# Kernel tuning notes

Hardware: AMD Instinct MI355X
Metric: run time of the kernel (lower is better)

## Reference

```python
import jax, jax.numpy as jnp
import numpy as np

N = 8192
C_IN = 512
C_INTER = 128  # in_channels // unit_nums = 512 // 4


def setup_inputs() -> dict:
    key = jax.random.key(0)
    ks = jax.random.split(key, 6)
    x = jax.random.normal(ks[0], (N, C_IN), dtype=jnp.float32)
    # Linear weights init: normal(0, 0.01); biases zero. Stored as [in, out].
    Wg = 0.01 * jax.random.normal(ks[1], (C_IN, C_INTER), dtype=jnp.float32)
    Wt = 0.01 * jax.random.normal(ks[2], (C_IN, C_INTER), dtype=jnp.float32)
    Wp = 0.01 * jax.random.normal(ks[3], (C_IN, C_INTER), dtype=jnp.float32)
    bg = jnp.zeros((C_INTER,), dtype=jnp.float32)
    bt = jnp.zeros((C_INTER,), dtype=jnp.float32)
    bp = jnp.zeros((C_INTER,), dtype=jnp.float32)
    # 1x1 conv weight (1, 2*C_INTER, 1, 1) flattened: first half hits theta, second half phi
    wcat = 0.01 * jax.random.normal(ks[4], (2 * C_INTER,), dtype=jnp.float32)
    return {"x": x, "Wg": Wg, "bg": bg, "Wt": Wt, "bt": bt, "Wp": Wp, "bp": bp, "wcat": wcat}


def reference(x, Wg, bg, Wt, bt, Wp, bp, wcat):
    n = x.shape[0]
    g_x = x @ Wg + bg          # [N, C_inter]
    theta = x @ Wt + bt        # [N, C_inter]
    phi = x @ Wp + bp          # [N, C_inter]
    c = theta.shape[1]
    # 1x1 conv over cat([theta_i, phi_j]) == w1.theta_i + w2.phi_j (outer sum), then ReLU
    a = theta @ wcat[:c]       # [N]
    b = phi @ wcat[c:]         # [N]
    f = jax.nn.relu(a[:, None] + b[None, :])  # [N, N]
    z = (f / n) @ g_x          # [N, C_inter]
    return z
```

## Files before the change

### kernel.cpp

```cpp
#include <hip/hip_runtime.h>

#define C_IN   512
#define C_INT  128
#define NBUCK  8192
#define SEG    32
#define NSEG   256

typedef short short8 __attribute__((ext_vector_type(8)));
typedef float floatx4 __attribute__((ext_vector_type(4)));


__device__ __forceinline__ int bucket_of(float v, float bmin, float inv_w) {
    float fk = (v - bmin) * inv_w;
    fk = fminf(fmaxf(fk, 0.f), (float)(NBUCK - 1));
    return (int)fk;
}

__device__ __forceinline__ short bf16rnd(float v) {
    unsigned u = __float_as_uint(v);
    return (short)((u + 0x7fffu + ((u >> 16) & 1u)) >> 16);
}


__global__ __launch_bounds__(256) void prep_kernel(
        const float* __restrict__ Wt, const float* __restrict__ Wp,
        const float* __restrict__ Wg, const float* __restrict__ wcat,
        const float* __restrict__ bt, const float* __restrict__ bp,
        float* __restrict__ ut, float* __restrict__ up, float* __restrict__ scal,
        unsigned short* __restrict__ WgT) {
    int t = threadIdx.x, bk = blockIdx.x;
    if (bk < 16) {
        const float* W  = (bk < 8) ? Wt : Wp;
        const float* wv = wcat + ((bk < 8) ? 0 : C_INT);
        float* dst      = (bk < 8) ? ut : up;
        int k = (bk & 7) * 64 + (t >> 2);
        int q = t & 3;
        const float4* row = (const float4*)(W + (size_t)k * C_INT);
        const float4* cv4 = (const float4*)wv;
        float s = 0.f;
        #pragma unroll
        for (int i = 0; i < 8; ++i) {
            float4 a = row[q * 8 + i];
            float4 c = cv4[q * 8 + i];
            s += a.x * c.x + a.y * c.y + a.z * c.z + a.w * c.w;
        }
        s += __shfl_xor(s, 1);
        s += __shfl_xor(s, 2);
        if (q == 0) dst[k] = s;
    } else if (bk == 16) {
        float s1p = (t < C_INT) ? bt[t] * wcat[t] : 0.f;
        float s2p = (t < C_INT) ? bp[t] * wcat[C_INT + t] : 0.f;
        for (int off = 32; off; off >>= 1) {
            s1p += __shfl_down(s1p, off);
            s2p += __shfl_down(s2p, off);
        }
        __shared__ float red[8];
        int w = t >> 6, lane = t & 63;
        if (lane == 0) { red[w] = s1p; red[4 + w] = s2p; }
        __syncthreads();
        if (t == 0) {
            scal[0] = red[0] + red[1] + red[2] + red[3];
            scal[1] = red[4] + red[5] + red[6] + red[7];
        }
    } else {
        __shared__ float tile[64][132];
        int kb = (bk - 17) * 64;
        #pragma unroll
        for (int it = 0; it < 8; ++it) {
            int idx = it * 256 + t;
            int r = idx >> 5, c4 = idx & 31;
            *(float4*)&tile[r][c4 * 4] =
                ((const float4*)(Wg + (size_t)(kb + r) * C_INT))[c4];
        }
        __syncthreads();
        int n = t & 127, kc = (t >> 7) * 32;
        unsigned pk[16];
        #pragma unroll
        for (int i = 0; i < 16; ++i) {
            unsigned lo = (unsigned short)bf16rnd(tile[kc + 2 * i][n]);
            unsigned hi = (unsigned short)bf16rnd(tile[kc + 2 * i + 1][n]);
            pk[i] = lo | (hi << 16);
        }
        uint4* dst = (uint4*)(WgT + (size_t)n * C_IN + kb + kc);
        #pragma unroll
        for (int i2 = 0; i2 < 4; ++i2) dst[i2] = *(uint4*)&pk[i2 * 4];
    }
}


#define RSTR 66

__global__ __launch_bounds__(256) void gemm_mfma(
        const float* __restrict__ x, const unsigned short* __restrict__ WgT,
        const float* __restrict__ bg,
        const float* __restrict__ ut, const float* __restrict__ up,
        const float* __restrict__ scal,
        _Float16* __restrict__ g, float* __restrict__ a, float* __restrict__ b) {
    __shared__ float red[3][20][RSTR];
    int tid = threadIdx.x;
    int lane = tid & 63, wv = tid >> 6;
    int bx = blockIdx.x;
    int i0 = (bx >> 1) * 16;
    int cg = bx & 1;
    int m = lane & 15, q = lane >> 4;
    floatx4 accg[4] = {};
    floatx4 accab = {};
    const float* xrow = x + (size_t)(i0 + m) * C_IN + q * 8;
    const float* absrc = (m == 0) ? ut : up;
    #pragma unroll
    for (int ks = 0; ks < 4; ++ks) {
        int k0 = (wv * 4 + ks) * 32;
        float4 f0 = *(const float4*)(xrow + k0);
        float4 f1 = *(const float4*)(xrow + k0 + 4);
        short8 af;
        af[0] = bf16rnd(f0.x); af[1] = bf16rnd(f0.y);
        af[2] = bf16rnd(f0.z); af[3] = bf16rnd(f0.w);
        af[4] = bf16rnd(f1.x); af[5] = bf16rnd(f1.y);
        af[6] = bf16rnd(f1.z); af[7] = bf16rnd(f1.w);
        if (cg == 0) {
            short8 abf = {};
            if (m < 2) {
                float4 u0 = *(const float4*)(absrc + k0 + q * 8);
                float4 u1 = *(const float4*)(absrc + k0 + q * 8 + 4);
                abf[0] = bf16rnd(u0.x); abf[1] = bf16rnd(u0.y);
                abf[2] = bf16rnd(u0.z); abf[3] = bf16rnd(u0.w);
                abf[4] = bf16rnd(u1.x); abf[5] = bf16rnd(u1.y);
                abf[6] = bf16rnd(u1.z); abf[7] = bf16rnd(u1.w);
            }
            accab = __builtin_amdgcn_mfma_f32_16x16x32_bf16(af, abf, accab, 0, 0, 0);
        }
        #pragma unroll
        for (int f = 0; f < 4; ++f) {
            short8 bfr = *(const short8*)(WgT + (size_t)(cg * 64 + f * 16 + m) * C_IN + k0 + q * 8);
            accg[f] = __builtin_amdgcn_mfma_f32_16x16x32_bf16(af, bfr, accg[f], 0, 0, 0);
        }
    }
    if (wv) {
        #pragma unroll
        for (int f = 0; f < 4; ++f)
            #pragma unroll
            for (int r = 0; r < 4; ++r)
                red[wv - 1][f * 4 + r][lane] = accg[f][r];
        #pragma unroll
        for (int r = 0; r < 4; ++r)
            red[wv - 1][16 + r][lane] = accab[r];
    }
    __syncthreads();
    if (wv == 0) {
        #pragma unroll
        for (int w = 0; w < 3; ++w) {
            #pragma unroll
            for (int f = 0; f < 4; ++f)
                #pragma unroll
                for (int r = 0; r < 4; ++r)
                    accg[f][r] += red[w][f * 4 + r][lane];
            #pragma unroll
            for (int r = 0; r < 4; ++r)
                accab[r] += red[w][16 + r][lane];
        }
        #pragma unroll
        for (int f = 0; f < 4; ++f) {
            int col = cg * 64 + f * 16 + m;
            float bgv = bg[col];
            #pragma unroll
            for (int r = 0; r < 4; ++r) {
                int row = i0 + q * 4 + r;
                g[(size_t)row * C_INT + col] = (_Float16)(accg[f][r] + bgv);
            }
        }
        if (cg == 0 && m < 2) {
            float off = m ? scal[1] : scal[0];
            float* dst = m ? b : a;
            #pragma unroll
            for (int r = 0; r < 4; ++r) dst[i0 + q * 4 + r] = accab[r] + off;
        }
    }
}


__global__ __launch_bounds__(1024) void sort_kernel(
        const float* __restrict__ b, float* __restrict__ scal,
        unsigned* __restrict__ offs_g, unsigned short* __restrict__ perm_g,
        float* __restrict__ bsort_g) {
    __shared__ unsigned oh[NBUCK / 2];
    __shared__ unsigned cur[NBUCK / 2];
    __shared__ unsigned short ls[8192];
    __shared__ unsigned wtu[16];
    __shared__ float smn[16], smx[16], sbp[2];
    int t = threadIdx.x, lane = t & 63, wv = t >> 6;
    #pragma unroll
    for (int r = 0; r < 4; ++r) { oh[t + r * 1024] = 0u; cur[t + r * 1024] = 0u; }
    float bv[8];
    float mn = 1e30f, mx = -1e30f;
    #pragma unroll
    for (int r = 0; r < 8; ++r) {
        bv[r] = b[t + r * 1024];
        mn = fminf(mn, bv[r]); mx = fmaxf(mx, bv[r]);
    }
    for (int off = 32; off; off >>= 1) {
        mn = fminf(mn, __shfl_down(mn, off));
        mx = fmaxf(mx, __shfl_down(mx, off));
    }
    if (lane == 0) { smn[wv] = mn; smx[wv] = mx; }
    __syncthreads();
    if (t == 0) {
        float gmn = smn[0], gmx = smx[0];
        #pragma unroll
        for (int i = 1; i < 16; ++i) {
            gmn = fminf(gmn, smn[i]); gmx = fmaxf(gmx, smx[i]);
        }
        float range = gmx - gmn;
        float iw = (range > 1e-30f) ? (float)NBUCK / range : 0.f;
        sbp[0] = gmn; sbp[1] = iw;
        scal[4] = gmn; scal[5] = iw;
    }
    __syncthreads();
    float bmin = sbp[0], inv_w = sbp[1];
    int kb[8];
    #pragma unroll
    for (int r = 0; r < 8; ++r) {
        kb[r] = bucket_of(bv[r], bmin, inv_w);
        atomicAdd(&oh[kb[r] >> 1], (kb[r] & 1) ? 0x10000u : 1u);
    }
    __syncthreads();
    unsigned h[8], p = 0;
    #pragma unroll
    for (int w = 0; w < 4; ++w) {
        unsigned word = oh[t * 4 + w];
        p += word & 0xffffu;  h[w * 2]     = p;
        p += word >> 16;      h[w * 2 + 1] = p;
    }
    unsigned v = p;
    #pragma unroll
    for (int d = 1; d < 64; d <<= 1) {
        unsigned u = __shfl_up(v, d);
        if (lane >= d) v += u;
    }
    if (lane == 63) wtu[wv] = v;
    __syncthreads();
    if (t < 16) {
        unsigned w = wtu[t];
        #pragma unroll
        for (int d = 1; d < 16; d <<= 1) {
            unsigned u = __shfl_up(w, d);
            if (t >= d) w += u;
        }
        wtu[t] = w;
    }
    __syncthreads();
    unsigned base = (v - p) + (wv ? wtu[wv - 1] : 0u);
    #pragma unroll
    for (int w = 0; w < 4; ++w) {
        unsigned lo = base + h[w * 2], hi = base + h[w * 2 + 1];
        oh[t * 4 + w] = lo | (hi << 16);
        offs_g[t * 8 + w * 2 + 1] = lo;
        offs_g[t * 8 + w * 2 + 2] = hi;
    }
    if (t == 0) offs_g[0] = 0u;
    __syncthreads();
    #pragma unroll
    for (int r = 0; r < 8; ++r) {
        int j = t + r * 1024;
        int k = kb[r];
        unsigned st = 0u;
        if (k > 0) {
            unsigned word = oh[(k - 1) >> 1];
            st = ((k - 1) & 1) ? (word >> 16) : (word & 0xffffu);
        }
        unsigned old = atomicAdd(&cur[k >> 1], (k & 1) ? 0x10000u : 1u);
        unsigned pos = (k & 1) ? (old >> 16) : (old & 0xffffu);
        ls[st + pos] = (unsigned short)j;
    }
    __syncthreads();
    #pragma unroll
    for (int r = 0; r < 8; ++r) {
        int e = t + r * 1024;
        int j = ls[e];
        perm_g[e] = (unsigned short)j;
        bsort_g[e] = b[j];
    }
}


__global__ __launch_bounds__(128) void segsum_kernel(
        const _Float16* __restrict__ g, const unsigned short* __restrict__ perm,
        const float* __restrict__ bsort,
        float* __restrict__ seg1, float* __restrict__ seg2) {
    __shared__ int pj[SEG];
    __shared__ float pb[SEG];
    int s = blockIdx.x, t = threadIdx.x;
    if (t < SEG) { pj[t] = perm[s * SEG + t]; pb[t] = bsort[s * SEG + t]; }
    __syncthreads();
    float a1 = 0.f, a2 = 0.f;
    #pragma unroll
    for (int e = 0; e < SEG; ++e) {
        float gv = (float)g[(size_t)pj[e] * C_INT + t];
        a1 += gv; a2 += pb[e] * gv;
    }
    seg1[s * C_INT + t] = a1;
    seg2[s * C_INT + t] = a2;
}


__global__ __launch_bounds__(128) void expand_kernel(
        const _Float16* __restrict__ g, const unsigned short* __restrict__ perm,
        const float* __restrict__ bsort,
        const float* __restrict__ seg1, const float* __restrict__ seg2,
        float* __restrict__ Pr1, float* __restrict__ Pr2) {
    __shared__ int pj[SEG];
    __shared__ float pb[SEG];
    int s = blockIdx.x, t = threadIdx.x;
    if (t < SEG) { pj[t] = perm[s * SEG + t]; pb[t] = bsort[s * SEG + t]; }
    __syncthreads();
    float r1 = 0.f, r2 = 0.f;
    for (int s2 = s + 1; s2 < NSEG; ++s2) {
        r1 += seg1[s2 * C_INT + t];
        r2 += seg2[s2 * C_INT + t];
    }
    #pragma unroll
    for (int e = SEG - 1; e >= 0; --e) {
        float gv = (float)g[(size_t)pj[e] * C_INT + t];
        r1 += gv; r2 += pb[e] * gv;
        size_t idx = (size_t)(s * SEG + e) * C_INT + t;
        Pr1[idx] = r1; Pr2[idx] = r2;
    }
    if (s == NSEG - 1) {
        Pr1[(size_t)8192 * C_INT + t] = 0.f;
        Pr2[(size_t)8192 * C_INT + t] = 0.f;
    }
}


__global__ __launch_bounds__(128) void out_kernel(
        const float* __restrict__ a, const float* __restrict__ scal,
        const _Float16* __restrict__ g,
        const unsigned* __restrict__ offs, const unsigned short* __restrict__ perm,
        const float* __restrict__ bsort,
        const float* __restrict__ Pr1, const float* __restrict__ Pr2,
        float* __restrict__ out, float inv_n) {
    __shared__ int pj[128];
    __shared__ float pb[128];
    int i = blockIdx.x, c = threadIdx.x;
    float ai = a[i], thr = -ai;
    float bmin = scal[4], inv_w = scal[5];
    int ki = bucket_of(thr, bmin, inv_w);
    unsigned e0 = offs[ki], e1 = offs[ki + 1];
    size_t base = (size_t)e1 * C_INT + c;
    float acc = ai * Pr1[base] + Pr2[base];
    for (unsigned be = e0; be < e1; be += 128) {
        unsigned cnt = min(128u, e1 - be);
        if ((unsigned)c < cnt) { pj[c] = perm[be + c]; pb[c] = bsort[be + c]; }
        __syncthreads();
        for (unsigned r = 0; r < cnt; ++r) {
            float bj = pb[r];
            if (bj > thr)
                acc += (ai + bj) * (float)g[(size_t)pj[r] * C_INT + c];
        }
        __syncthreads();
    }
    out[(size_t)i * C_INT + c] = acc * inv_n;
}


extern "C" void kernel_launch(void* const* d_in, const int* in_sizes, int n_in,
                              void* d_out, int out_size, void* d_ws, size_t ws_size,
                              hipStream_t stream) {
    const float* x    = (const float*)d_in[0];
    const float* Wg   = (const float*)d_in[1];
    const float* bg   = (const float*)d_in[2];
    const float* Wt   = (const float*)d_in[3];
    const float* bt   = (const float*)d_in[4];
    const float* Wp   = (const float*)d_in[5];
    const float* bp   = (const float*)d_in[6];
    const float* wcat = (const float*)d_in[7];
    float* out = (float*)d_out;
    int n = in_sizes[0] / C_IN;

    char* w = (char*)d_ws;
    size_t off = 0;
    auto alloc = [&](size_t bytes) -> void* {
        void* p = w + off;
        off += (bytes + 255) & ~(size_t)255;
        return p;
    };
    float*          ut    = (float*)alloc(C_IN * 4);
    float*          up    = (float*)alloc(C_IN * 4);
    float*          scal  = (float*)alloc(32);
    float*          a     = (float*)alloc((size_t)n * 4);
    float*          b     = (float*)alloc((size_t)n * 4);
    unsigned*       offs  = (unsigned*)alloc((size_t)(NBUCK + 1) * 4);
    unsigned short* perm  = (unsigned short*)alloc((size_t)n * 2);
    float*          bsort = (float*)alloc((size_t)n * 4);
    _Float16*       g     = (_Float16*)alloc((size_t)n * C_INT * 2);
    unsigned short* WgT   = (unsigned short*)alloc((size_t)C_INT * C_IN * 2);
    float*          seg1  = (float*)alloc((size_t)NSEG * C_INT * 4);
    float*          seg2  = (float*)alloc((size_t)NSEG * C_INT * 4);
    float*          Pr1   = (float*)alloc((size_t)(n + 1) * C_INT * 4);
    float*          Pr2   = (float*)alloc((size_t)(n + 1) * C_INT * 4);

    prep_kernel<<<25, 256, 0, stream>>>(Wt, Wp, Wg, wcat, bt, bp, ut, up, scal, WgT);
    gemm_mfma<<<n / 8, 256, 0, stream>>>(x, WgT, bg, ut, up, scal, g, a, b);
    sort_kernel<<<1, 1024, 0, stream>>>(b, scal, offs, perm, bsort);
    segsum_kernel<<<NSEG, 128, 0, stream>>>(g, perm, bsort, seg1, seg2);
    expand_kernel<<<NSEG, 128, 0, stream>>>(g, perm, bsort, seg1, seg2, Pr1, Pr2);
    out_kernel<<<n, 128, 0, stream>>>(a, scal, g, offs, perm, bsort, Pr1, Pr2,
                                      out, 1.0f / (float)n);
}
```

Baseline: 142.7 us.

## Fuse sort, segment-sum and expand kernels into one persistent kernel with grid barriers

```diff
diff --git a/kernel.cpp b/kernel.cpp
--- a/kernel.cpp
+++ b/kernel.cpp
@@ -27,7 +27,7 @@
         const float* __restrict__ Wg, const float* __restrict__ wcat,
         const float* __restrict__ bt, const float* __restrict__ bp,
         float* __restrict__ ut, float* __restrict__ up, float* __restrict__ scal,
-        unsigned short* __restrict__ WgT) {
+        unsigned short* __restrict__ WgT, unsigned* __restrict__ sync) {
     int t = threadIdx.x, bk = blockIdx.x;
     if (bk < 16) {
         const float* W  = (bk < 8) ? Wt : Wp;
@@ -61,6 +61,7 @@
         if (t == 0) {
             scal[0] = red[0] + red[1] + red[2] + red[3];
             scal[1] = red[4] + red[5] + red[6] + red[7];
+            sync[0] = 0u; sync[1] = 0u;
         }
     } else {
         __shared__ float tile[64][132];
@@ -178,153 +179,185 @@
 }
 
 
-__global__ __launch_bounds__(1024) void sort_kernel(
-        const float* __restrict__ b, float* __restrict__ scal,
+__global__ __launch_bounds__(1024) void post1_kernel(
+        const _Float16* __restrict__ g, const float* __restrict__ b,
+        float* __restrict__ scal,
         unsigned* __restrict__ offs_g, unsigned short* __restrict__ perm_g,
-        float* __restrict__ bsort_g) {
-    __shared__ unsigned oh[NBUCK / 2];
-    __shared__ unsigned cur[NBUCK / 2];
-    __shared__ unsigned short ls[8192];
-    __shared__ unsigned wtu[16];
-    __shared__ float smn[16], smx[16], sbp[2];
-    int t = threadIdx.x, lane = t & 63, wv = t >> 6;
-    #pragma unroll
-    for (int r = 0; r < 4; ++r) { oh[t + r * 1024] = 0u; cur[t + r * 1024] = 0u; }
-    float bv[8];
-    float mn = 1e30f, mx = -1e30f;
-    #pragma unroll
-    for (int r = 0; r < 8; ++r) {
-        bv[r] = b[t + r * 1024];
-        mn = fminf(mn, bv[r]); mx = fmaxf(mx, bv[r]);
-    }
-    for (int off = 32; off; off >>= 1) {
-        mn = fminf(mn, __shfl_down(mn, off));
-        mx = fmaxf(mx, __shfl_down(mx, off));
-    }
-    if (lane == 0) { smn[wv] = mn; smx[wv] = mx; }
-    __syncthreads();
-    if (t == 0) {
-        float gmn = smn[0], gmx = smx[0];
-        #pragma unroll
-        for (int i = 1; i < 16; ++i) {
-            gmn = fminf(gmn, smn[i]); gmx = fmaxf(gmx, smx[i]);
-        }
-        float range = gmx - gmn;
-        float iw = (range > 1e-30f) ? (float)NBUCK / range : 0.f;
-        sbp[0] = gmn; sbp[1] = iw;
-        scal[4] = gmn; scal[5] = iw;
-    }
-    __syncthreads();
-    float bmin = sbp[0], inv_w = sbp[1];
-    int kb[8];
-    #pragma unroll
-    for (int r = 0; r < 8; ++r) {
-        kb[r] = bucket_of(bv[r], bmin, inv_w);
-        atomicAdd(&oh[kb[r] >> 1], (kb[r] & 1) ? 0x10000u : 1u);
-    }
-    __syncthreads();
-    unsigned h[8], p = 0;
-    #pragma unroll
-    for (int w = 0; w < 4; ++w) {
-        unsigned word = oh[t * 4 + w];
-        p += word & 0xffffu;  h[w * 2]     = p;
-        p += word >> 16;      h[w * 2 + 1] = p;
-    }
-    unsigned v = p;
-    #pragma unroll
-    for (int d = 1; d < 64; d <<= 1) {
-        unsigned u = __shfl_up(v, d);
-        if (lane >= d) v += u;
-    }
-    if (lane == 63) wtu[wv] = v;
-    __syncthreads();
-    if (t < 16) {
-        unsigned w = wtu[t];
-        #pragma unroll
-        for (int d = 1; d < 16; d <<= 1) {
-            unsigned u = __shfl_up(w, d);
-            if (t >= d) w += u;
-        }
-        wtu[t] = w;
-    }
-    __syncthreads();
-    unsigned base = (v - p) + (wv ? wtu[wv - 1] : 0u);
-    #pragma unroll
-    for (int w = 0; w < 4; ++w) {
-        unsigned lo = base + h[w * 2], hi = base + h[w * 2 + 1];
-        oh[t * 4 + w] = lo | (hi << 16);
-        offs_g[t * 8 + w * 2 + 1] = lo;
-        offs_g[t * 8 + w * 2 + 2] = hi;
-    }
-    if (t == 0) offs_g[0] = 0u;
-    __syncthreads();
-    #pragma unroll
-    for (int r = 0; r < 8; ++r) {
-        int j = t + r * 1024;
-        int k = kb[r];
-        unsigned st = 0u;
-        if (k > 0) {
-            unsigned word = oh[(k - 1) >> 1];
-            st = ((k - 1) & 1) ? (word >> 16) : (word & 0xffffu);
-        }
-        unsigned old = atomicAdd(&cur[k >> 1], (k & 1) ? 0x10000u : 1u);
-        unsigned pos = (k & 1) ? (old >> 16) : (old & 0xffffu);
-        ls[st + pos] = (unsigned short)j;
-    }
-    __syncthreads();
-    #pragma unroll
-    for (int r = 0; r < 8; ++r) {
-        int e = t + r * 1024;
-        int j = ls[e];
-        perm_g[e] = (unsigned short)j;
-        bsort_g[e] = b[j];
-    }
-}
-
-
-__global__ __launch_bounds__(128) void segsum_kernel(
-        const _Float16* __restrict__ g, const unsigned short* __restrict__ perm,
-        const float* __restrict__ bsort,
-        float* __restrict__ seg1, float* __restrict__ seg2) {
-    __shared__ int pj[SEG];
-    __shared__ float pb[SEG];
-    int s = blockIdx.x, t = threadIdx.x;
-    if (t < SEG) { pj[t] = perm[s * SEG + t]; pb[t] = bsort[s * SEG + t]; }
-    __syncthreads();
+        float* __restrict__ bsort_g,
+        float* __restrict__ seg1, float* __restrict__ seg2,
+        float* __restrict__ Pr1, float* __restrict__ Pr2,
+        unsigned* __restrict__ sync) {
+    __shared__ __align__(16) unsigned char smem[49408];
+    unsigned*       oh  = (unsigned*)(smem);
+    unsigned*       cur = (unsigned*)(smem + 16384);
+    unsigned short* ls  = (unsigned short*)(smem + 32768);
+    unsigned*       wtu = (unsigned*)(smem + 49152);
+    float*          smn = (float*)(smem + 49216);
+    float*          smx = (float*)(smem + 49280);
+    float* part1 = (float*)(smem);
+    float* part2 = (float*)(smem + 4096);
+    float* rs1   = (float*)(smem + 8192);
+    float* rs2   = (float*)(smem + 12288);
+    int*   pj    = (int*)(smem + 16384);
+    float* pb    = (float*)(smem + 16512);
+
+    int t = threadIdx.x, s = blockIdx.x;
+    int lane = t & 63, wv = t >> 6;
+
+    if (s == 0) {
+        #pragma unroll
+        for (int r = 0; r < 4; ++r) { oh[t + r * 1024] = 0u; cur[t + r * 1024] = 0u; }
+        float bv[8];
+        float mn = 1e30f, mx = -1e30f;
+        #pragma unroll
+        for (int r = 0; r < 8; ++r) {
+            bv[r] = b[t + r * 1024];
+            mn = fminf(mn, bv[r]); mx = fmaxf(mx, bv[r]);
+        }
+        for (int off = 32; off; off >>= 1) {
+            mn = fminf(mn, __shfl_down(mn, off));
+            mx = fmaxf(mx, __shfl_down(mx, off));
+        }
+        if (lane == 0) { smn[wv] = mn; smx[wv] = mx; }
+        __syncthreads();
+        if (t == 0) {
+            float gmn = smn[0], gmx = smx[0];
+            #pragma unroll
+            for (int i = 1; i < 16; ++i) {
+                gmn = fminf(gmn, smn[i]); gmx = fmaxf(gmx, smx[i]);
+            }
+            float range = gmx - gmn;
+            float iw = (range > 1e-30f) ? (float)NBUCK / range : 0.f;
+            smn[0] = gmn; smx[0] = iw;
+            scal[4] = gmn; scal[5] = iw;
+        }
+        __syncthreads();
+        float bmin = smn[0], inv_w = smx[0];
+        int kb[8];
+        #pragma unroll
+        for (int r = 0; r < 8; ++r) {
+            kb[r] = bucket_of(bv[r], bmin, inv_w);
+            atomicAdd(&oh[kb[r] >> 1], (kb[r] & 1) ? 0x10000u : 1u);
+        }
+        __syncthreads();
+        unsigned h[8], p = 0;
+        #pragma unroll
+        for (int w = 0; w < 4; ++w) {
+            unsigned word = oh[t * 4 + w];
+            p += word & 0xffffu;  h[w * 2]     = p;
+            p += word >> 16;      h[w * 2 + 1] = p;
+        }
+        unsigned v = p;
+        #pragma unroll
+        for (int d = 1; d < 64; d <<= 1) {
+            unsigned u = __shfl_up(v, d);
+            if (lane >= d) v += u;
+        }
+        if (lane == 63) wtu[wv] = v;
+        __syncthreads();
+        if (t < 16) {
+            unsigned w = wtu[t];
+            #pragma unroll
+            for (int d = 1; d < 16; d <<= 1) {
+                unsigned u = __shfl_up(w, d);
+                if (t >= d) w += u;
+            }
+            wtu[t] = w;
+        }
+        __syncthreads();
+        unsigned base = (v - p) + (wv ? wtu[wv - 1] : 0u);
+        #pragma unroll
+        for (int w = 0; w < 4; ++w) {
+            unsigned lo = base + h[w * 2], hi = base + h[w * 2 + 1];
+            oh[t * 4 + w] = lo | (hi << 16);
+            offs_g[t * 8 + w * 2 + 1] = lo;
+            offs_g[t * 8 + w * 2 + 2] = hi;
+        }
+        if (t == 0) offs_g[0] = 0u;
+        __syncthreads();
+        #pragma unroll
+        for (int r = 0; r < 8; ++r) {
+            int j = t + r * 1024;
+            int k = kb[r];
+            unsigned st = 0u;
+            if (k > 0) {
+                unsigned word = oh[(k - 1) >> 1];
+                st = ((k - 1) & 1) ? (word >> 16) : (word & 0xffffu);
+            }
+            unsigned old = atomicAdd(&cur[k >> 1], (k & 1) ? 0x10000u : 1u);
+            unsigned pos = (k & 1) ? (old >> 16) : (old & 0xffffu);
+            ls[st + pos] = (unsigned short)j;
+        }
+        __syncthreads();
+        #pragma unroll
+        for (int r = 0; r < 8; ++r) {
+            int e = t + r * 1024;
+            int j = ls[e];
+            perm_g[e] = (unsigned short)j;
+            bsort_g[e] = b[j];
+        }
+        __threadfence();
+        __syncthreads();
+        if (t == 0) atomicAdd(&sync[0], 1u);
+    }
+    if (t == 0) { while (atomicAdd(&sync[0], 0u) == 0u) {} }
+    __syncthreads();
+    __threadfence();
+
+    int c = t & 127, p = t >> 7;
+    if (t < SEG) { pj[t] = perm_g[s * SEG + t]; pb[t] = bsort_g[s * SEG + t]; }
+    __syncthreads();
+
     float a1 = 0.f, a2 = 0.f;
     #pragma unroll
-    for (int e = 0; e < SEG; ++e) {
-        float gv = (float)g[(size_t)pj[e] * C_INT + t];
+    for (int e = p * 4; e < p * 4 + 4; ++e) {
+        float gv = (float)g[(size_t)pj[e] * C_INT + c];
         a1 += gv; a2 += pb[e] * gv;
     }
-    seg1[s * C_INT + t] = a1;
-    seg2[s * C_INT + t] = a2;
-}
-
-
-__global__ __launch_bounds__(128) void expand_kernel(
-        const _Float16* __restrict__ g, const unsigned short* __restrict__ perm,
-        const float* __restrict__ bsort,
-        const float* __restrict__ seg1, const float* __restrict__ seg2,
-        float* __restrict__ Pr1, float* __restrict__ Pr2) {
-    __shared__ int pj[SEG];
-    __shared__ float pb[SEG];
-    int s = blockIdx.x, t = threadIdx.x;
-    if (t < SEG) { pj[t] = perm[s * SEG + t]; pb[t] = bsort[s * SEG + t]; }
-    __syncthreads();
+    part1[p * 128 + c] = a1; part2[p * 128 + c] = a2;
+    __syncthreads();
+    if (p == 0) {
+        float t1 = 0.f, t2 = 0.f;
+        #pragma unroll
+        for (int pp = 0; pp < 8; ++pp) {
+            t1 += part1[pp * 128 + c]; t2 += part2[pp * 128 + c];
+        }
+        seg1[s * C_INT + c] = t1; seg2[s * C_INT + c] = t2;
+        __threadfence();
+    }
+    __syncthreads();
+    if (t == 0) {
+        atomicAdd(&sync[1], 1u);
+        while (atomicAdd(&sync[1], 0u) < (unsigned)NSEG) {}
+    }
+    __syncthreads();
+    __threadfence();
+
     float r1 = 0.f, r2 = 0.f;
-    for (int s2 = s + 1; s2 < NSEG; ++s2) {
-        r1 += seg1[s2 * C_INT + t];
-        r2 += seg2[s2 * C_INT + t];
-    }
+    for (int s2 = s + 1 + p; s2 < NSEG; s2 += 8) {
+        r1 += seg1[s2 * C_INT + c];
+        r2 += seg2[s2 * C_INT + c];
+    }
+    rs1[p * 128 + c] = r1; rs2[p * 128 + c] = r2;
+    __syncthreads();
+    float rseg1 = 0.f, rseg2 = 0.f;
     #pragma unroll
-    for (int e = SEG - 1; e >= 0; --e) {
-        float gv = (float)g[(size_t)pj[e] * C_INT + t];
-        r1 += gv; r2 += pb[e] * gv;
-        size_t idx = (size_t)(s * SEG + e) * C_INT + t;
-        Pr1[idx] = r1; Pr2[idx] = r2;
-    }
-    if (s == NSEG - 1) {
+    for (int pp = 0; pp < 8; ++pp) {
+        rseg1 += rs1[pp * 128 + c]; rseg2 += rs2[pp * 128 + c];
+    }
+    float w1 = rseg1, w2 = rseg2;
+    #pragma unroll
+    for (int pp = p + 1; pp < 8; ++pp) {
+        w1 += part1[pp * 128 + c]; w2 += part2[pp * 128 + c];
+    }
+    #pragma unroll
+    for (int e = p * 4 + 3; e >= p * 4; --e) {
+        float gv = (float)g[(size_t)pj[e] * C_INT + c];
+        w1 += gv; w2 += pb[e] * gv;
+        size_t idx = (size_t)(s * SEG + e) * C_INT + c;
+        Pr1[idx] = w1; Pr2[idx] = w2;
+    }
+    if (s == 0 && t < C_INT) {
         Pr1[(size_t)8192 * C_INT + t] = 0.f;
         Pr2[(size_t)8192 * C_INT + t] = 0.f;
     }
@@ -386,6 +419,7 @@
     float*          ut    = (float*)alloc(C_IN * 4);
     float*          up    = (float*)alloc(C_IN * 4);
     float*          scal  = (float*)alloc(32);
+    unsigned*       sync  = (unsigned*)alloc(16);
     float*          a     = (float*)alloc((size_t)n * 4);
     float*          b     = (float*)alloc((size_t)n * 4);
     unsigned*       offs  = (unsigned*)alloc((size_t)(NBUCK + 1) * 4);
@@ -398,11 +432,11 @@
     float*          Pr1   = (float*)alloc((size_t)(n + 1) * C_INT * 4);
     float*          Pr2   = (float*)alloc((size_t)(n + 1) * C_INT * 4);
 
-    prep_kernel<<<25, 256, 0, stream>>>(Wt, Wp, Wg, wcat, bt, bp, ut, up, scal, WgT);
+    prep_kernel<<<25, 256, 0, stream>>>(Wt, Wp, Wg, wcat, bt, bp, ut, up, scal,
+                                        WgT, sync);
     gemm_mfma<<<n / 8, 256, 0, stream>>>(x, WgT, bg, ut, up, scal, g, a, b);
-    sort_kernel<<<1, 1024, 0, stream>>>(b, scal, offs, perm, bsort);
-    segsum_kernel<<<NSEG, 128, 0, stream>>>(g, perm, bsort, seg1, seg2);
-    expand_kernel<<<NSEG, 128, 0, stream>>>(g, perm, bsort, seg1, seg2, Pr1, Pr2);
+    post1_kernel<<<NSEG, 1024, 0, stream>>>(g, b, scal, offs, perm, bsort,
+                                            seg1, seg2, Pr1, Pr2, sync);
     out_kernel<<<n, 128, 0, stream>>>(a, scal, g, offs, perm, bsort, Pr1, Pr2,
                                       out, 1.0f / (float)n);
 }
```

After: 254.3 us. +78.1%, slower.

## Fuse sort and segment sums by redundantly sorting in every block

Applied to the files above, without the earlier changes.

```diff
diff --git a/kernel.cpp b/kernel.cpp
--- a/kernel.cpp
+++ b/kernel.cpp
@@ -3,8 +3,8 @@
 #define C_IN   512
 #define C_INT  128
 #define NBUCK  8192
-#define SEG    32
 #define NSEG   256
+#define BPS    (NBUCK / NSEG)
 
 typedef short short8 __attribute__((ext_vector_type(8)));
 typedef float floatx4 __attribute__((ext_vector_type(4)));
@@ -178,16 +178,20 @@
 }
 
 
-__global__ __launch_bounds__(1024) void sort_kernel(
-        const float* __restrict__ b, float* __restrict__ scal,
+__global__ __launch_bounds__(1024) void postA_kernel(
+        const _Float16* __restrict__ g, const float* __restrict__ b,
+        float* __restrict__ scal,
         unsigned* __restrict__ offs_g, unsigned short* __restrict__ perm_g,
-        float* __restrict__ bsort_g) {
+        float* __restrict__ bsort_g,
+        float* __restrict__ seg1, float* __restrict__ seg2) {
     __shared__ unsigned oh[NBUCK / 2];
     __shared__ unsigned cur[NBUCK / 2];
     __shared__ unsigned short ls[8192];
     __shared__ unsigned wtu[16];
-    __shared__ float smn[16], smx[16], sbp[2];
-    int t = threadIdx.x, lane = t & 63, wv = t >> 6;
+    __shared__ float smn[16], smx[16];
+    __shared__ float part1[8][128], part2[8][128];
+    int t = threadIdx.x, s = blockIdx.x;
+    int lane = t & 63, wv = t >> 6;
     #pragma unroll
     for (int r = 0; r < 4; ++r) { oh[t + r * 1024] = 0u; cur[t + r * 1024] = 0u; }
     float bv[8];
@@ -211,11 +215,11 @@
         }
         float range = gmx - gmn;
         float iw = (range > 1e-30f) ? (float)NBUCK / range : 0.f;
-        sbp[0] = gmn; sbp[1] = iw;
-        scal[4] = gmn; scal[5] = iw;
-    }
-    __syncthreads();
-    float bmin = sbp[0], inv_w = sbp[1];
+        smn[0] = gmn; smx[0] = iw;
+        if (s == 0) { scal[4] = gmn; scal[5] = iw; }
+    }
+    __syncthreads();
+    float bmin = smn[0], inv_w = smx[0];
     int kb[8];
     #pragma unroll
     for (int r = 0; r < 8; ++r) {
@@ -223,14 +227,14 @@
         atomicAdd(&oh[kb[r] >> 1], (kb[r] & 1) ? 0x10000u : 1u);
     }
     __syncthreads();
-    unsigned h[8], p = 0;
+    unsigned h[8], p0 = 0;
     #pragma unroll
     for (int w = 0; w < 4; ++w) {
         unsigned word = oh[t * 4 + w];
-        p += word & 0xffffu;  h[w * 2]     = p;
-        p += word >> 16;      h[w * 2 + 1] = p;
-    }
-    unsigned v = p;
+        p0 += word & 0xffffu;  h[w * 2]     = p0;
+        p0 += word >> 16;      h[w * 2 + 1] = p0;
+    }
+    unsigned v = p0;
     #pragma unroll
     for (int d = 1; d < 64; d <<= 1) {
         unsigned u = __shfl_up(v, d);
@@ -248,15 +252,17 @@
         wtu[t] = w;
     }
     __syncthreads();
-    unsigned base = (v - p) + (wv ? wtu[wv - 1] : 0u);
+    unsigned base = (v - p0) + (wv ? wtu[wv - 1] : 0u);
     #pragma unroll
     for (int w = 0; w < 4; ++w) {
         unsigned lo = base + h[w * 2], hi = base + h[w * 2 + 1];
         oh[t * 4 + w] = lo | (hi << 16);
-        offs_g[t * 8 + w * 2 + 1] = lo;
-        offs_g[t * 8 + w * 2 + 2] = hi;
-    }
-    if (t == 0) offs_g[0] = 0u;
+        if (s == 0) {
+            offs_g[t * 8 + w * 2 + 1] = lo;
+            offs_g[t * 8 + w * 2 + 2] = hi;
+        }
+    }
+    if (s == 0 && t == 0) offs_g[0] = 0u;
     __syncthreads();
     #pragma unroll
     for (int r = 0; r < 8; ++r) {
@@ -272,61 +278,68 @@
         ls[st + pos] = (unsigned short)j;
     }
     __syncthreads();
-    #pragma unroll
-    for (int r = 0; r < 8; ++r) {
-        int e = t + r * 1024;
+    auto incl = [&](int kk) -> unsigned {
+        unsigned word = oh[kk >> 1];
+        return (kk & 1) ? (word >> 16) : (word & 0xffffu);
+    };
+    unsigned E0 = (s == 0) ? 0u : incl(s * BPS - 1);
+    unsigned E1 = incl((s + 1) * BPS - 1);
+    for (unsigned e = E0 + t; e < E1; e += 1024) {
         int j = ls[e];
         perm_g[e] = (unsigned short)j;
         bsort_g[e] = b[j];
     }
-}
-
-
-__global__ __launch_bounds__(128) void segsum_kernel(
-        const _Float16* __restrict__ g, const unsigned short* __restrict__ perm,
-        const float* __restrict__ bsort,
-        float* __restrict__ seg1, float* __restrict__ seg2) {
-    __shared__ int pj[SEG];
-    __shared__ float pb[SEG];
-    int s = blockIdx.x, t = threadIdx.x;
-    if (t < SEG) { pj[t] = perm[s * SEG + t]; pb[t] = bsort[s * SEG + t]; }
-    __syncthreads();
+    int c = t & 127, p = t >> 7;
     float a1 = 0.f, a2 = 0.f;
-    #pragma unroll
-    for (int e = 0; e < SEG; ++e) {
-        float gv = (float)g[(size_t)pj[e] * C_INT + t];
-        a1 += gv; a2 += pb[e] * gv;
-    }
-    seg1[s * C_INT + t] = a1;
-    seg2[s * C_INT + t] = a2;
-}
-
-
-__global__ __launch_bounds__(128) void expand_kernel(
-        const _Float16* __restrict__ g, const unsigned short* __restrict__ perm,
-        const float* __restrict__ bsort,
+    for (unsigned e = E0 + p; e < E1; e += 8) {
+        int j = ls[e];
+        float gv = (float)g[(size_t)j * C_INT + c];
+        a1 += gv; a2 += b[j] * gv;
+    }
+    part1[p][c] = a1; part2[p][c] = a2;
+    __syncthreads();
+    if (p == 0) {
+        float t1 = 0.f, t2 = 0.f;
+        #pragma unroll
+        for (int pp = 0; pp < 8; ++pp) { t1 += part1[pp][c]; t2 += part2[pp][c]; }
+        seg1[s * C_INT + c] = t1;
+        seg2[s * C_INT + c] = t2;
+    }
+}
+
+
+__global__ __launch_bounds__(128) void postB_kernel(
+        const _Float16* __restrict__ g, const unsigned* __restrict__ offs,
+        const unsigned short* __restrict__ perm, const float* __restrict__ bsort,
         const float* __restrict__ seg1, const float* __restrict__ seg2,
         float* __restrict__ Pr1, float* __restrict__ Pr2) {
-    __shared__ int pj[SEG];
-    __shared__ float pb[SEG];
-    int s = blockIdx.x, t = threadIdx.x;
-    if (t < SEG) { pj[t] = perm[s * SEG + t]; pb[t] = bsort[s * SEG + t]; }
-    __syncthreads();
+    __shared__ int pj[128];
+    __shared__ float pb[128];
+    int s = blockIdx.x, c = threadIdx.x;
+    unsigned E0 = offs[s * BPS], E1 = offs[(s + 1) * BPS];
     float r1 = 0.f, r2 = 0.f;
     for (int s2 = s + 1; s2 < NSEG; ++s2) {
-        r1 += seg1[s2 * C_INT + t];
-        r2 += seg2[s2 * C_INT + t];
-    }
-    #pragma unroll
-    for (int e = SEG - 1; e >= 0; --e) {
-        float gv = (float)g[(size_t)pj[e] * C_INT + t];
-        r1 += gv; r2 += pb[e] * gv;
-        size_t idx = (size_t)(s * SEG + e) * C_INT + t;
-        Pr1[idx] = r1; Pr2[idx] = r2;
-    }
-    if (s == NSEG - 1) {
-        Pr1[(size_t)8192 * C_INT + t] = 0.f;
-        Pr2[(size_t)8192 * C_INT + t] = 0.f;
+        r1 += seg1[s2 * C_INT + c];
+        r2 += seg2[s2 * C_INT + c];
+    }
+    unsigned e = E1;
+    while (e > E0) {
+        unsigned cb = (e >= E0 + 128u) ? e - 128u : E0;
+        unsigned cnt = e - cb;
+        if ((unsigned)c < cnt) { pj[c] = perm[cb + c]; pb[c] = bsort[cb + c]; }
+        __syncthreads();
+        for (int r = (int)cnt - 1; r >= 0; --r) {
+            float gv = (float)g[(size_t)pj[r] * C_INT + c];
+            r1 += gv; r2 += pb[r] * gv;
+            size_t idx = (size_t)(cb + r) * C_INT + c;
+            Pr1[idx] = r1; Pr2[idx] = r2;
+        }
+        __syncthreads();
+        e = cb;
+    }
+    if (s == 0) {
+        Pr1[(size_t)8192 * C_INT + c] = 0.f;
+        Pr2[(size_t)8192 * C_INT + c] = 0.f;
     }
 }
 
@@ -400,9 +413,8 @@
 
     prep_kernel<<<25, 256, 0, stream>>>(Wt, Wp, Wg, wcat, bt, bp, ut, up, scal, WgT);
     gemm_mfma<<<n / 8, 256, 0, stream>>>(x, WgT, bg, ut, up, scal, g, a, b);
-    sort_kernel<<<1, 1024, 0, stream>>>(b, scal, offs, perm, bsort);
-    segsum_kernel<<<NSEG, 128, 0, stream>>>(g, perm, bsort, seg1, seg2);
-    expand_kernel<<<NSEG, 128, 0, stream>>>(g, perm, bsort, seg1, seg2, Pr1, Pr2);
+    postA_kernel<<<NSEG, 1024, 0, stream>>>(g, b, scal, offs, perm, bsort, seg1, seg2);
+    postB_kernel<<<NSEG, 128, 0, stream>>>(g, offs, perm, bsort, seg1, seg2, Pr1, Pr2);
     out_kernel<<<n, 128, 0, stream>>>(a, scal, g, offs, perm, bsort, Pr1, Pr2,
                                       out, 1.0f / (float)n);
 }
```

Result: no change. 143.5 us (+0.5%).
